# Kernel tuning notes

Hardware: AMD Instinct MI355X
Metric: run time of the kernel (lower is better)

The kernel has to match this reference:

```python
import jax, jax.numpy as jnp
import numpy as np

N, E, D = 100000, 400000, 128

def setup_inputs() -> dict:
    key = jax.random.key(0)
    k1, k2, k3, k4, k5 = jax.random.split(key, 5)
    x = jax.random.normal(k1, (N, D), dtype=jnp.float32)
    e = jax.random.normal(k2, (E, D), dtype=jnp.float32)
    # torch nn.Linear(3D, D, bias=False) weight is [D, 3D]; we store W = weight.T -> [3D, D]
    W = jax.random.normal(k3, (3 * D, D), dtype=jnp.float32) * (1.0 / np.sqrt(3 * D))
    src_idx = jax.random.randint(k4, (E,), 0, N, dtype=jnp.int64)
    dst_idx = jax.random.randint(k5, (E,), 0, N, dtype=jnp.int64)
    return {"x": x, "e": e, "W": W, "src_idx": src_idx, "dst_idx": dst_idx}

def reference(x, e, W, src_idx, dst_idx):
    # message = Linear(concat([src_feat, tgt_feat, role_feat], -1))
    # Split W into the three d-blocks so we never materialize the [E, 3D] concat:
    # concat([a,b,c]) @ W == a@W1 + b@W2 + c@W3  (exactly the same math)
    d = x.shape[-1]
    W_src, W_dst, W_e = W[:d], W[d:2 * d], W[2 * d:]
    m = x[src_idx] @ W_src + x[dst_idx] @ W_dst + e @ W_e  # [E, D]
    return m
```

## Files before the change

### kernel.cpp

```cpp
#include <hip/hip_runtime.h>
#include <hip/hip_bf16.h>

typedef __attribute__((ext_vector_type(8))) short bf16x8;
typedef __attribute__((ext_vector_type(4))) float f32x4;

#define D128 128
#define TILE_M 128
#define LDW 136
#define WCHUNK (D128 * LDW)
#define XB_OFF (131072 / 2)

__device__ __forceinline__ short f2bf(float f) {
    union { float f; unsigned u; } v; v.f = f;
    unsigned r = (v.u + 0x7FFFu + ((v.u >> 16) & 1u)) >> 16;
    return (short)r;
}

__device__ __forceinline__ short f2bf_h(float f) {
    __hip_bfloat16 h = __float2bfloat16(f);
    short s;
    __builtin_memcpy(&s, &h, sizeof(short));
    return s;
}

__device__ __forceinline__ bf16x8 pack8(float4 a, float4 b) {
    bf16x8 r;
    r[0] = f2bf_h(a.x); r[1] = f2bf_h(a.y); r[2] = f2bf_h(a.z); r[3] = f2bf_h(a.w);
    r[4] = f2bf_h(b.x); r[5] = f2bf_h(b.y); r[6] = f2bf_h(b.z); r[7] = f2bf_h(b.w);
    return r;
}

__device__ __forceinline__ void gload_lds16(const short* g, short* l) {
    __builtin_amdgcn_global_load_lds(
        (const __attribute__((address_space(1))) unsigned int*)(const void*)g,
        (__attribute__((address_space(3))) unsigned int*)(void*)l, 16, 0, 0);
}

__global__ __launch_bounds__(256) void wt_kernel(const float* __restrict__ W,
                                                 short* __restrict__ WTp) {
    const int c  = blockIdx.x >> 4;
    const int n0 = (blockIdx.x & 15) * 8;
    const int tid = threadIdx.x;
#pragma unroll
    for (int i = 0; i < 4; ++i) {
        int li = i * 256 + tid;
        int nn = li >> 7;
        int k  = li & 127;
        float v = W[(size_t)(c * 128 + k) * D128 + (n0 + nn)];
        WTp[(size_t)c * WCHUNK + (size_t)(n0 + nn) * LDW + k] = f2bf(v);
    }
}

__global__ __launch_bounds__(256) void xb_kernel(const float* __restrict__ x,
                                                 short* __restrict__ xb) {
    const size_t i = ((size_t)blockIdx.x * 256 + threadIdx.x) * 8;
    float4 v0 = reinterpret_cast<const float4*>(x + i)[0];
    float4 v1 = reinterpret_cast<const float4*>(x + i)[1];
    *reinterpret_cast<bf16x8*>(xb + i) = pack8(v0, v1);
}

__global__ __launch_bounds__(512, 4) void fused_kernel(
        const short* __restrict__ xb,
        const float* __restrict__ e,
        const short* __restrict__ WTp,
        const int*  __restrict__ src_idx,
        const int*  __restrict__ dst_idx,
        float* __restrict__ out)
{
    __shared__ short Ws[2][WCHUNK];

    const int tid  = threadIdx.x;
    const int r0   = blockIdx.x * TILE_M;
    const int w    = tid >> 6;
    const int lane = tid & 63;
    const int lrow = lane & 15;
    const int lhi  = lane >> 4;
    const int arow = w * 16 + lrow;

    const int si = src_idx[r0 + arow];
    const int di = dst_idx[r0 + arow];
    const short* xrow_s = xb + (size_t)si * D128;
    const short* xrow_d = xb + (size_t)di * D128;
    const float* erow   = e + (size_t)(r0 + arow) * D128;

    f32x4 acc[8];
#pragma unroll
    for (int n = 0; n < 8; ++n) acc[n] = (f32x4){0.f, 0.f, 0.f, 0.f};

    auto stageB = [&](short* dstbuf, const short* srcw) {
        const int base = w * 64;
#pragma unroll
        for (int j = 0; j < 4; ++j) {
            int unit = j * 512 + base;
            gload_lds16(srcw + (size_t)(unit + lane) * 8, dstbuf + (size_t)unit * 8);
        }
        if (w < 2) {
            int unit = 2048 + base;
            gload_lds16(srcw + (size_t)(unit + lane) * 8, dstbuf + (size_t)unit * 8);
        }
    };
    auto loadA_x = [&](bf16x8 a[4], const short* rowp) {
#pragma unroll
        for (int ks = 0; ks < 4; ++ks)
            a[ks] = *reinterpret_cast<const bf16x8*>(rowp + ks * 32 + lhi * 8);
    };
    auto mfma_phase = [&](const bf16x8 a[4], const short* Wbuf) {
#pragma unroll
        for (int ks = 0; ks < 4; ++ks)
#pragma unroll
            for (int n = 0; n < 8; ++n) {
                bf16x8 b = *reinterpret_cast<const bf16x8*>(
                    &Wbuf[(n * 16 + lrow) * LDW + ks * 32 + lhi * 8]);
                acc[n] = __builtin_amdgcn_mfma_f32_16x16x32_bf16(a[ks], b, acc[n], 0, 0, 0);
            }
    };

    stageB(Ws[0], WTp);
    asm volatile("" ::: "memory");
    bf16x8 a_cur[4];
    loadA_x(a_cur, xrow_s);
    asm volatile("s_waitcnt vmcnt(4)" ::: "memory");
    __builtin_amdgcn_s_barrier();

    stageB(Ws[1], WTp + WCHUNK);
    asm volatile("" ::: "memory");
    bf16x8 a_nxt[4];
    loadA_x(a_nxt, xrow_d);
    mfma_phase(a_cur, Ws[0]);
    asm volatile("s_waitcnt vmcnt(4)" ::: "memory");
    __builtin_amdgcn_s_barrier();

    stageB(Ws[0], WTp + 2 * WCHUNK);
    asm volatile("" ::: "memory");
    float4 ev[8];
#pragma unroll
    for (int ks = 0; ks < 4; ++ks) {
        ev[2 * ks]     = reinterpret_cast<const float4*>(erow + ks * 32 + lhi * 8)[0];
        ev[2 * ks + 1] = reinterpret_cast<const float4*>(erow + ks * 32 + lhi * 8)[1];
    }
    mfma_phase(a_nxt, Ws[1]);
    asm volatile("s_waitcnt vmcnt(8)" ::: "memory");
    __builtin_amdgcn_s_barrier();

    bf16x8 a_e[4];
#pragma unroll
    for (int ks = 0; ks < 4; ++ks) a_e[ks] = pack8(ev[2 * ks], ev[2 * ks + 1]);
    mfma_phase(a_e, Ws[0]);

#pragma unroll
    for (int n = 0; n < 8; ++n)
#pragma unroll
        for (int j = 0; j < 4; ++j) {
            int row = r0 + w * 16 + lhi * 4 + j;
            int col = n * 16 + lrow;
            out[(size_t)row * D128 + col] = acc[n][j];
        }
}

extern "C" void kernel_launch(void* const* d_in, const int* in_sizes, int n_in,
                              void* d_out, int out_size, void* d_ws, size_t ws_size,
                              hipStream_t stream) {
    const float* x = (const float*)d_in[0];
    const float* e = (const float*)d_in[1];
    const float* W = (const float*)d_in[2];
    const int* src = (const int*)d_in[3];
    const int* dst = (const int*)d_in[4];
    float* out = (float*)d_out;

    short* WTp = (short*)d_ws;
    short* xb  = (short*)d_ws + XB_OFF;

    const int N = in_sizes[0] / D128;
    const int E = in_sizes[3];
    const int blocks = E / TILE_M;

    wt_kernel<<<48, 256, 0, stream>>>(W, WTp);
    xb_kernel<<<(N * D128) / (256 * 8), 256, 0, stream>>>(x, xb);
    fused_kernel<<<blocks, 512, 0, stream>>>(xb, e, WTp, src, dst, out);
}
```

Baseline: 136.9 us.

## Swap MFMA operand roles with pre-fragmented weight image and vectorized stores

Pre-packs the three weight blocks into an MFMA-fragment-ordered bf16 image so each lane reads its A operand from LDS as one contiguous 16-byte load, free of bank conflicts and padding. The weights become the A operand and the gathered rows the B operand, so each lane's accumulators hold four consecutive output columns. This allows float4 output stores instead of scalar strided ones. The tile grows to 256 rows with 1024 threads, all three weight chunks are loaded into LDS at once, and every activation load is issued up front with a single barrier. A bounds guard handles a ragged final tile. The larger 96KB LDS footprint and 1024-thread blocks may limit occupancy and latency hiding.

```diff
diff --git a/kernel.cpp b/kernel.cpp
--- a/kernel.cpp
+++ b/kernel.cpp
@@ -5,9 +5,8 @@
 typedef __attribute__((ext_vector_type(4))) float f32x4;
 
 #define D128 128
-#define TILE_M 128
-#define LDW 136
-#define WCHUNK (D128 * LDW)
+#define TILE_M 256
+#define IMG_SHORTS 16384
 #define XB_OFF (131072 / 2)
 
 __device__ __forceinline__ short f2bf(float f) {
@@ -37,18 +36,19 @@
 }
 
 __global__ __launch_bounds__(256) void wt_kernel(const float* __restrict__ W,
-                                                 short* __restrict__ WTp) {
-    const int c  = blockIdx.x >> 4;
-    const int n0 = (blockIdx.x & 15) * 8;
-    const int tid = threadIdx.x;
+                                                 short* __restrict__ Wimg) {
+    const int c    = blockIdx.x >> 3;
+    const int frag = (blockIdx.x & 7) * 4 + (threadIdx.x >> 6);
+    const int lane = threadIdx.x & 63;
+    const int mt = frag >> 2, ks = frag & 3;
+    const int m  = mt * 16 + (lane & 15);
+    const int k0 = ks * 32 + (lane >> 4) * 8;
+    bf16x8 v;
 #pragma unroll
-    for (int i = 0; i < 4; ++i) {
-        int li = i * 256 + tid;
-        int nn = li >> 7;
-        int k  = li & 127;
-        float v = W[(size_t)(c * 128 + k) * D128 + (n0 + nn)];
-        WTp[(size_t)c * WCHUNK + (size_t)(n0 + nn) * LDW + k] = f2bf(v);
-    }
+    for (int j = 0; j < 8; ++j)
+        v[j] = f2bf(W[(size_t)(c * 128 + k0 + j) * D128 + m]);
+    *reinterpret_cast<bf16x8*>(
+        &Wimg[((size_t)c * 32 + frag) * 64 * 8 + (size_t)lane * 8]) = v;
 }
 
 __global__ __launch_bounds__(256) void xb_kernel(const float* __restrict__ x,
@@ -59,102 +59,92 @@
     *reinterpret_cast<bf16x8*>(xb + i) = pack8(v0, v1);
 }
 
-__global__ __launch_bounds__(512, 4) void fused_kernel(
+__global__ __launch_bounds__(1024, 4) void fused_kernel(
         const short* __restrict__ xb,
         const float* __restrict__ e,
-        const short* __restrict__ WTp,
+        const short* __restrict__ Wimg,
         const int*  __restrict__ src_idx,
         const int*  __restrict__ dst_idx,
-        float* __restrict__ out)
+        float* __restrict__ out,
+        int E)
 {
-    __shared__ short Ws[2][WCHUNK];
+    __shared__ short Ws[3 * IMG_SHORTS];
 
     const int tid  = threadIdx.x;
+    const int lane = tid & 63;
+    const int w    = tid >> 6;
+    const int lhi  = lane >> 4;
     const int r0   = blockIdx.x * TILE_M;
-    const int w    = tid >> 6;
-    const int lane = tid & 63;
-    const int lrow = lane & 15;
-    const int lhi  = lane >> 4;
-    const int arow = w * 16 + lrow;
+    const int rn   = r0 + w * 16 + (lane & 15);
+    const bool valid = rn < E;
+    const int  rl  = valid ? rn : (E - 1);
 
-    const int si = src_idx[r0 + arow];
-    const int di = dst_idx[r0 + arow];
-    const short* xrow_s = xb + (size_t)si * D128;
-    const short* xrow_d = xb + (size_t)di * D128;
-    const float* erow   = e + (size_t)(r0 + arow) * D128;
+    const int si = src_idx[rl];
+    const int di = dst_idx[rl];
+    asm volatile("" ::: "memory");
+
+#pragma unroll
+    for (int jj = 0; jj < 6; ++jj) {
+        int unit = jj * 1024 + tid;
+        gload_lds16(Wimg + (size_t)unit * 8, &Ws[unit * 8]);
+    }
+    asm volatile("" ::: "memory");
+
+    const short* ps = xb + (size_t)si * D128;
+    const short* pd = xb + (size_t)di * D128;
+    const float* pe = e + (size_t)rl * D128;
+    bf16x8 bs[4], bd[4];
+    float4 ev[8];
+#pragma unroll
+    for (int ks = 0; ks < 4; ++ks) {
+        bs[ks] = *reinterpret_cast<const bf16x8*>(ps + ks * 32 + lhi * 8);
+        bd[ks] = *reinterpret_cast<const bf16x8*>(pd + ks * 32 + lhi * 8);
+        ev[2 * ks]     = reinterpret_cast<const float4*>(pe + ks * 32 + lhi * 8)[0];
+        ev[2 * ks + 1] = reinterpret_cast<const float4*>(pe + ks * 32 + lhi * 8)[1];
+    }
+    asm volatile("" ::: "memory");
+    asm volatile("s_waitcnt vmcnt(16)" ::: "memory");
+    __builtin_amdgcn_s_barrier();
 
     f32x4 acc[8];
 #pragma unroll
-    for (int n = 0; n < 8; ++n) acc[n] = (f32x4){0.f, 0.f, 0.f, 0.f};
-
-    auto stageB = [&](short* dstbuf, const short* srcw) {
-        const int base = w * 64;
-#pragma unroll
-        for (int j = 0; j < 4; ++j) {
-            int unit = j * 512 + base;
-            gload_lds16(srcw + (size_t)(unit + lane) * 8, dstbuf + (size_t)unit * 8);
-        }
-        if (w < 2) {
-            int unit = 2048 + base;
-            gload_lds16(srcw + (size_t)(unit + lane) * 8, dstbuf + (size_t)unit * 8);
-        }
-    };
-    auto loadA_x = [&](bf16x8 a[4], const short* rowp) {
-#pragma unroll
-        for (int ks = 0; ks < 4; ++ks)
-            a[ks] = *reinterpret_cast<const bf16x8*>(rowp + ks * 32 + lhi * 8);
-    };
-    auto mfma_phase = [&](const bf16x8 a[4], const short* Wbuf) {
-#pragma unroll
-        for (int ks = 0; ks < 4; ++ks)
-#pragma unroll
-            for (int n = 0; n < 8; ++n) {
-                bf16x8 b = *reinterpret_cast<const bf16x8*>(
-                    &Wbuf[(n * 16 + lrow) * LDW + ks * 32 + lhi * 8]);
-                acc[n] = __builtin_amdgcn_mfma_f32_16x16x32_bf16(a[ks], b, acc[n], 0, 0, 0);
-            }
-    };
-
-    stageB(Ws[0], WTp);
-    asm volatile("" ::: "memory");
-    bf16x8 a_cur[4];
-    loadA_x(a_cur, xrow_s);
-    asm volatile("s_waitcnt vmcnt(4)" ::: "memory");
-    __builtin_amdgcn_s_barrier();
-
-    stageB(Ws[1], WTp + WCHUNK);
-    asm volatile("" ::: "memory");
-    bf16x8 a_nxt[4];
-    loadA_x(a_nxt, xrow_d);
-    mfma_phase(a_cur, Ws[0]);
-    asm volatile("s_waitcnt vmcnt(4)" ::: "memory");
-    __builtin_amdgcn_s_barrier();
-
-    stageB(Ws[0], WTp + 2 * WCHUNK);
-    asm volatile("" ::: "memory");
-    float4 ev[8];
-#pragma unroll
-    for (int ks = 0; ks < 4; ++ks) {
-        ev[2 * ks]     = reinterpret_cast<const float4*>(erow + ks * 32 + lhi * 8)[0];
-        ev[2 * ks + 1] = reinterpret_cast<const float4*>(erow + ks * 32 + lhi * 8)[1];
-    }
-    mfma_phase(a_nxt, Ws[1]);
-    asm volatile("s_waitcnt vmcnt(8)" ::: "memory");
-    __builtin_amdgcn_s_barrier();
-
-    bf16x8 a_e[4];
-#pragma unroll
-    for (int ks = 0; ks < 4; ++ks) a_e[ks] = pack8(ev[2 * ks], ev[2 * ks + 1]);
-    mfma_phase(a_e, Ws[0]);
+    for (int mt = 0; mt < 8; ++mt) acc[mt] = (f32x4){0.f, 0.f, 0.f, 0.f};
 
 #pragma unroll
-    for (int n = 0; n < 8; ++n)
+    for (int ks = 0; ks < 4; ++ks)
 #pragma unroll
-        for (int j = 0; j < 4; ++j) {
-            int row = r0 + w * 16 + lhi * 4 + j;
-            int col = n * 16 + lrow;
-            out[(size_t)row * D128 + col] = acc[n][j];
+        for (int mt = 0; mt < 8; ++mt) {
+            bf16x8 a = *reinterpret_cast<const bf16x8*>(
+                &Ws[((0 * 32 + mt * 4 + ks) * 64 + lane) * 8]);
+            acc[mt] = __builtin_amdgcn_mfma_f32_16x16x32_bf16(a, bs[ks], acc[mt], 0, 0, 0);
         }
+#pragma unroll
+    for (int ks = 0; ks < 4; ++ks)
+#pragma unroll
+        for (int mt = 0; mt < 8; ++mt) {
+            bf16x8 a = *reinterpret_cast<const bf16x8*>(
+                &Ws[((1 * 32 + mt * 4 + ks) * 64 + lane) * 8]);
+            acc[mt] = __builtin_amdgcn_mfma_f32_16x16x32_bf16(a, bd[ks], acc[mt], 0, 0, 0);
+        }
+
+    bf16x8 be[4];
+#pragma unroll
+    for (int ks = 0; ks < 4; ++ks) be[ks] = pack8(ev[2 * ks], ev[2 * ks + 1]);
+#pragma unroll
+    for (int ks = 0; ks < 4; ++ks)
+#pragma unroll
+        for (int mt = 0; mt < 8; ++mt) {
+            bf16x8 a = *reinterpret_cast<const bf16x8*>(
+                &Ws[((2 * 32 + mt * 4 + ks) * 64 + lane) * 8]);
+            acc[mt] = __builtin_amdgcn_mfma_f32_16x16x32_bf16(a, be[ks], acc[mt], 0, 0, 0);
+        }
+
+    if (valid) {
+        float* po = out + (size_t)rn * D128 + lhi * 4;
+#pragma unroll
+        for (int mt = 0; mt < 8; ++mt)
+            *reinterpret_cast<float4*>(po + mt * 16) = *(float4*)&acc[mt];
+    }
 }
 
 extern "C" void kernel_launch(void* const* d_in, const int* in_sizes, int n_in,
@@ -167,14 +157,14 @@
     const int* dst = (const int*)d_in[4];
     float* out = (float*)d_out;
 
-    short* WTp = (short*)d_ws;
-    short* xb  = (short*)d_ws + XB_OFF;
+    short* Wimg = (short*)d_ws;
+    short* xb   = (short*)d_ws + XB_OFF;
 
     const int N = in_sizes[0] / D128;
     const int E = in_sizes[3];
-    const int blocks = E / TILE_M;
+    const int blocks = (E + TILE_M - 1) / TILE_M;
 
-    wt_kernel<<<48, 256, 0, stream>>>(W, WTp);
+    wt_kernel<<<24, 256, 0, stream>>>(W, Wimg);
     xb_kernel<<<(N * D128) / (256 * 8), 256, 0, stream>>>(x, xb);
-    fused_kernel<<<blocks, 512, 0, stream>>>(xb, e, WTp, src, dst, out);
+    fused_kernel<<<blocks, 1024, 0, stream>>>(xb, e, Wimg, src, dst, out, E);
 }
```

New measurement: 165.6 us. +21.0%, slower.
